# Kernel optimization log

Hardware: AMD Instinct MI355X
Metric: run time of the kernel (lower is better)

Reference implementation:

```python
import jax, jax.numpy as jnp
import numpy as np

N_CH = 128      # n_channels (out_channels)
MID = 128       # mid_channels
NF = 16         # num_filters
N_NODES = 50000


def _omeg():
    i = jnp.arange(NF, dtype=jnp.float32)
    return (10.0 * N_CH ** (1.0 - 2.0 * i / NF)).reshape(1, NF)


def setup_inputs() -> dict:
    key = jax.random.key(0)
    ks = jax.random.split(key, 16)
    E = 800000
    inp = {
        "x": jax.random.normal(ks[0], (N_NODES, N_CH), jnp.float32),
        "edge_index": jax.random.randint(ks[1], (2, E), 0, N_NODES, jnp.int64),
        "edge_attr": jax.random.normal(ks[2], (E, N_CH), jnp.float32),
        "x_pos": jax.random.normal(ks[3], (N_NODES, 3), jnp.float32),
    }
    def lin(k, fan_in, fan_out):
        kw, kb = jax.random.split(k)
        bound = 1.0 / np.sqrt(fan_in)
        w = jax.random.uniform(kw, (fan_in, fan_out), jnp.float32, -bound, bound)
        b = jax.random.uniform(kb, (fan_out,), jnp.float32, -bound, bound)
        return w, b
    inp["w1"], inp["b1"] = lin(ks[4], N_CH, N_CH)          # atomwise1
    inp["mw1"], inp["mb1"] = lin(ks[5], 2 * NF + 2 * N_CH, MID)  # message MLP
    inp["mw2"], inp["mb2"] = lin(ks[6], MID, MID)
    inp["mw3"], inp["mb3"] = lin(ks[7], MID, N_CH)
    inp["w2"], inp["b2"] = lin(ks[8], N_CH, N_CH)          # atomwise2
    inp["w3"], inp["b3"] = lin(ks[9], N_CH, N_CH)          # atomwise3
    return inp


def reference(x, edge_index, edge_attr, x_pos, w1, b1, mw1, mb1, mw2, mb2, mw3, mb3, w2, b2, w3, b3):
    h = x @ w1 + b1                                   # atomwise1 [N, C]
    src, dst = edge_index[0], edge_index[1]           # PyG: x_j = src, x_i = dst
    r = jnp.linalg.norm(x_pos[dst] - x_pos[src], axis=-1, keepdims=True)  # [E,1], p=2
    feat = r * _omeg()                                # [E, NF]
    msg_in = jnp.concatenate([jnp.sin(feat), jnp.cos(feat), edge_attr, h[src]], axis=-1)
    m = jax.nn.gelu(msg_in @ mw1 + mb1, approximate=False)
    m = jax.nn.gelu(m @ mw2 + mb2, approximate=False)
    m = m @ mw3 + mb3                                 # dropout is identity at eval
    agg = jax.ops.segment_sum(m, dst, num_segments=N_NODES)
    h = h + agg                                       # residual in cfconv
    out = jax.nn.relu(h @ w2 + b2) @ w3 + b3
    return out
```

## Files before the change

kernel.cpp:

```cpp
#include <hip/hip_runtime.h>
#include <math.h>

#define NCH 128
#define TE 64
#define TF 32
#define AP 296
#define AF 132
#define XP 136

typedef __attribute__((ext_vector_type(8))) _Float16 half8;
typedef __attribute__((ext_vector_type(4))) _Float16 half4;
typedef __attribute__((ext_vector_type(4))) float f32x4;

__device__ __forceinline__ float gelu_exact(float v) {
    return 0.5f * v * (1.0f + erff(v * 0.70710678118654752f));
}

__device__ __forceinline__ float erf_fast(float x) {
    float ax = fabsf(x);
    float t  = __builtin_amdgcn_rcpf(fmaf(0.3275911f, ax, 1.0f));
    float p  = fmaf(t, 1.061405429f, -1.453152027f);
    p = fmaf(t, p, 1.421413741f);
    p = fmaf(t, p, -0.284496736f);
    p = fmaf(t, p, 0.254829592f);
    float e  = exp2f(-ax * ax * 1.4426950408889634f);
    float r  = fmaf(-p * t, e, 1.0f);
    return copysignf(r, x);
}

__device__ __forceinline__ float gelu_fast(float v) {
    return 0.5f * v * (1.0f + erf_fast(v * 0.70710678118654752f));
}

__device__ __forceinline__ half4 cvt4(float4 v) {
#if __has_builtin(__builtin_amdgcn_cvt_pkrtz)
    auto a = __builtin_amdgcn_cvt_pkrtz(v.x, v.y);
    auto b = __builtin_amdgcn_cvt_pkrtz(v.z, v.w);
    half4 r;
    r[0] = a[0]; r[1] = a[1]; r[2] = b[0]; r[3] = b[1];
    return r;
#else
    return (half4){(_Float16)v.x, (_Float16)v.y, (_Float16)v.z, (_Float16)v.w};
#endif
}

__device__ __forceinline__ void sincos_rev(float rev, float* s, float* c) {
    float fr = rev - floorf(rev);
#if __has_builtin(__builtin_amdgcn_sinf) && __has_builtin(__builtin_amdgcn_cosf)
    *s = __builtin_amdgcn_sinf(fr);
    *c = __builtin_amdgcn_cosf(fr);
#else
    float rad = fr * 6.283185307179586f;
    *s = sinf(rad);
    *c = cosf(rad);
#endif
}

__global__ __launch_bounds__(256) void k_hist(const int* __restrict__ ei,
                                              int* __restrict__ cnt, int E) {
    int e = blockIdx.x * 256 + threadIdx.x;
    if (e < E) atomicAdd(&cnt[ei[E + e]], 1);
}

__global__ __launch_bounds__(256) void k_scan_local(const int* __restrict__ cnt,
                                                    int* __restrict__ fill,
                                                    int* __restrict__ bsum, int n) {
    __shared__ int sdata[256];
    const int tid = threadIdx.x;
    const int i = blockIdx.x * 256 + tid;
    int v = (i < n) ? cnt[i] : 0;
    sdata[tid] = v;
    __syncthreads();
    #pragma unroll
    for (int off = 1; off < 256; off <<= 1) {
        int t = (tid >= off) ? sdata[tid - off] : 0;
        __syncthreads();
        sdata[tid] += t;
        __syncthreads();
    }
    if (i < n) fill[i] = sdata[tid] - v;
    if (tid == 255) bsum[blockIdx.x] = sdata[255];
}

__global__ __launch_bounds__(256) void k_scan_bsum(int* __restrict__ bsum, int nb) {
    __shared__ int sdata[256];
    const int tid = threadIdx.x;
    int v = (tid < nb) ? bsum[tid] : 0;
    sdata[tid] = v;
    __syncthreads();
    #pragma unroll
    for (int off = 1; off < 256; off <<= 1) {
        int t = (tid >= off) ? sdata[tid - off] : 0;
        __syncthreads();
        sdata[tid] += t;
        __syncthreads();
    }
    if (tid < nb) bsum[tid] = sdata[tid] - v;
}

__global__ __launch_bounds__(256) void k_scan_add(int* __restrict__ fill,
                                                  const int* __restrict__ bsum, int n) {
    int i = blockIdx.x * 256 + threadIdx.x;
    if (i < n) fill[i] += bsum[blockIdx.x];
}

__global__ __launch_bounds__(256) void k_scan_serial(const int* __restrict__ cnt,
                                                     int* __restrict__ fill, int n) {
    __shared__ int sdata[256];
    __shared__ int carry;
    const int tid = threadIdx.x;
    if (tid == 0) carry = 0;
    __syncthreads();
    for (int base = 0; base < n; base += 256) {
        int i = base + tid;
        int v = (i < n) ? cnt[i] : 0;
        sdata[tid] = v;
        __syncthreads();
        #pragma unroll
        for (int off = 1; off < 256; off <<= 1) {
            int t = (tid >= off) ? sdata[tid - off] : 0;
            __syncthreads();
            sdata[tid] += t;
            __syncthreads();
        }
        int incl = sdata[tid];
        if (i < n) fill[i] = incl - v + carry;
        __syncthreads();
        if (tid == 255) carry += incl;
        __syncthreads();
    }
}

__global__ __launch_bounds__(256) void k_permute(const int* __restrict__ ei,
                                                 int* __restrict__ fill,
                                                 int* __restrict__ perm, int E) {
    int e = blockIdx.x * 256 + threadIdx.x;
    if (e < E) {
        int d = ei[E + e];
        int slot = atomicAdd(&fill[d], 1);
        perm[slot] = e;
    }
}

__global__ __launch_bounds__(256) void k_prep_all(
    const float* __restrict__ mw1, const float* __restrict__ mw2,
    const float* __restrict__ mw3, const float* __restrict__ w1,
    const float* __restrict__ w2, const float* __restrict__ w3,
    _Float16* __restrict__ wf, _Float16* __restrict__ awf,
    _Float16* __restrict__ o2f, _Float16* __restrict__ o3f)
{
    int b = blockIdx.x;
    const float* W; _Float16* out; int nch;
    if      (b < 18) { W = mw1; out = wf;             nch = 9; }
    else if (b < 26) { W = mw2; out = wf + 9 * 4096;  nch = 4; b -= 18; }
    else if (b < 34) { W = mw3; out = wf + 13 * 4096; nch = 4; b -= 26; }
    else if (b < 42) { W = w1;  out = awf;            nch = 4; b -= 34; }
    else if (b < 50) { W = w2;  out = o2f;            nch = 4; b -= 42; }
    else             { W = w3;  out = o3f;            nch = 4; b -= 50; }
    int idx = b * 256 + threadIdx.x;
    if (idx >= nch * 512) return;
    int c    = idx >> 9;
    int r    = idx & 511;
    int wv   = r >> 7;
    int nf   = (r >> 6) & 1;
    int lane = r & 63;
    int n  = wv * 32 + nf * 16 + (lane & 15);
    int k0 = c * 32 + (lane >> 4) * 8;
    half8 v;
    #pragma unroll
    for (int j = 0; j < 8; ++j) v[j] = (_Float16)W[(size_t)(k0 + j) * NCH + n];
    *(half8*)(out + (size_t)idx * 8) = v;
}

__global__ __launch_bounds__(256, 4) void k_aw1_mfma(
    const float* __restrict__ x, const _Float16* __restrict__ awf,
    const float* __restrict__ b1, float* __restrict__ h,
    _Float16* __restrict__ h2, int N)
{
    __shared__ __align__(16) _Float16 Xs[64][XP];

    const int tid  = threadIdx.x;
    const int row0 = blockIdx.x * 64;
    const int lane = tid & 63;
    const int w    = tid >> 6;
    const int lrow = lane & 15;
    const int lk8  = lane >> 4;
    const int n0   = w * 32;

    const half8* bp = (const half8*)awf + (w * 128 + lane);
    half8 b[2][2];
    b[0][0] = bp[0];   b[0][1] = bp[64];
    b[1][0] = bp[512]; b[1][1] = bp[512 + 64];

    #pragma unroll
    for (int t = 0; t < 8; ++t) {
        int idx = tid + t * 256;
        int r = idx >> 5, f4 = idx & 31;
        int gr = row0 + r;
        float4 v = {0.f, 0.f, 0.f, 0.f};
        if (gr < N) v = *(const float4*)(x + (size_t)gr * NCH + f4 * 4);
        *(half4*)&Xs[r][f4 * 4] = cvt4(v);
    }
    __syncthreads();

    f32x4 acc[4][2];
    #pragma unroll
    for (int mb = 0; mb < 4; ++mb)
        #pragma unroll
        for (int nf = 0; nf < 2; ++nf) acc[mb][nf] = (f32x4){0.f, 0.f, 0.f, 0.f};

    #pragma unroll
    for (int i = 0; i < 4; ++i) {
        const int s = i & 1;
        half8 av[4];
        #pragma unroll
        for (int mb = 0; mb < 4; ++mb)
            av[mb] = *(const half8*)&Xs[mb * 16 + lrow][i * 32 + lk8 * 8];
        #pragma unroll
        for (int mb = 0; mb < 4; ++mb) {
            acc[mb][0] = __builtin_amdgcn_mfma_f32_16x16x32_f16(av[mb], b[s][0], acc[mb][0], 0, 0, 0);
            acc[mb][1] = __builtin_amdgcn_mfma_f32_16x16x32_f16(av[mb], b[s][1], acc[mb][1], 0, 0, 0);
        }
        if (i + 2 < 4) {
            b[s][0] = bp[(size_t)(i + 2) * 512];
            b[s][1] = bp[(size_t)(i + 2) * 512 + 64];
        }
    }

    float bi0 = b1[n0 + lrow], bi1 = b1[n0 + 16 + lrow];
    #pragma unroll
    for (int mb = 0; mb < 4; ++mb)
        #pragma unroll
        for (int q = 0; q < 4; ++q) {
            int gr = row0 + mb * 16 + lk8 * 4 + q;
            if (gr < N) {
                float v0 = acc[mb][0][q] + bi0;
                float v1 = acc[mb][1][q] + bi1;
                h[(size_t)gr * NCH + n0 + lrow]       = v0;
                h[(size_t)gr * NCH + n0 + 16 + lrow]  = v1;
                h2[(size_t)gr * NCH + n0 + lrow]      = (_Float16)v0;
                h2[(size_t)gr * NCH + n0 + 16 + lrow] = (_Float16)v1;
            }
        }
}

__global__ __launch_bounds__(256, 8) void k_edges_mfma(
    const int* __restrict__ ei, const float* __restrict__ eattr,
    const float* __restrict__ xpos, const _Float16* __restrict__ h2,
    float* h,
    const int* __restrict__ perm,
    const _Float16* __restrict__ wf,
    const float* __restrict__ mb1, const float* __restrict__ mb2,
    const float* __restrict__ mb3, int E)
{
    __shared__ __align__(16) _Float16 As[TF][AP];
    __shared__ int permS[TF], dstS[TF];

    const int tid  = threadIdx.x;
    const int e0   = blockIdx.x * TF;
    const int lane = tid & 63;
    const int w    = tid >> 6;
    const int lrow = lane & 15;
    const int lk8  = lane >> 4;
    const int n0   = w * 32;

    const half8* bp = (const half8*)wf + (w * 128 + lane);
    half8 b[2][2];
    b[0][0] = bp[0];   b[0][1] = bp[64];
    b[1][0] = bp[512]; b[1][1] = bp[512 + 64];

    if (tid < TF) {
        int ge = e0 + tid;
        int pe = (ge < E) ? perm[ge] : -1;
        permS[tid] = pe;
        dstS[tid]  = (pe >= 0) ? ei[E + pe] : -1;
    }
    __syncthreads();

    float4 ea[4];
    #pragma unroll
    for (int t = 0; t < 4; ++t) {
        int idx = tid + t * 256;
        int pe = permS[idx >> 5];
        ea[t] = (pe >= 0) ? *(const float4*)(eattr + (size_t)pe * NCH + (idx & 31) * 4)
                          : (float4){0.f, 0.f, 0.f, 0.f};
    }
    uint4 hv[2];
    #pragma unroll
    for (int t = 0; t < 2; ++t) {
        int idx = tid + t * 256;
        int pe = permS[idx >> 4];
        int s = (pe >= 0) ? ei[pe] : 0;
        hv[t] = *(const uint4*)(h2 + (size_t)s * NCH + (idx & 15) * 8);
    }

    {
        int le = tid >> 3, i0 = tid & 7;
        int pe = permS[le];
        float r = 0.f;
        if (pe >= 0) {
            int s = ei[pe], d = dstS[le];
            float dx = xpos[d * 3 + 0] - xpos[s * 3 + 0];
            float dy = xpos[d * 3 + 1] - xpos[s * 3 + 1];
            float dz = xpos[d * 3 + 2] - xpos[s * 3 + 2];
            r = sqrtf(dx * dx + dy * dy + dz * dz);
        }
        #pragma unroll
        for (int u = 0; u < 2; ++u) {
            int i = i0 + u * 8;
            float omr = 1.5915494309f * exp2f(7.0f - 0.875f * (float)i);
            float sv, cv;
            sincos_rev(r * omr, &sv, &cv);
            As[le][i]      = (_Float16)sv;
            As[le][16 + i] = (_Float16)cv;
        }
    }
    #pragma unroll
    for (int t = 0; t < 4; ++t) {
        int idx = tid + t * 256;
        *(half4*)&As[idx >> 5][32 + (idx & 31) * 4] = cvt4(ea[t]);
    }
    #pragma unroll
    for (int t = 0; t < 2; ++t) {
        int idx = tid + t * 256;
        *(uint4*)&As[idx >> 4][160 + (idx & 15) * 8] = hv[t];
    }
    __syncthreads();

    f32x4 acc[2][2];
    #pragma unroll
    for (int mb = 0; mb < 2; ++mb)
        #pragma unroll
        for (int nf = 0; nf < 2; ++nf) acc[mb][nf] = (f32x4){0.f, 0.f, 0.f, 0.f};

    auto epi = [&](const float* __restrict__ mbv) {
        float bi0 = mbv[n0 + lrow], bi1 = mbv[n0 + 16 + lrow];
        #pragma unroll
        for (int mb = 0; mb < 2; ++mb)
            #pragma unroll
            for (int nf = 0; nf < 2; ++nf) {
                float bb = nf ? bi1 : bi0;
                #pragma unroll
                for (int q = 0; q < 4; ++q) {
                    float g = gelu_fast(acc[mb][nf][q] + bb);
                    As[mb * 16 + lk8 * 4 + q][n0 + nf * 16 + lrow] = (_Float16)g;
                }
                acc[mb][nf] = (f32x4){0.f, 0.f, 0.f, 0.f};
            }
    };

    #pragma unroll
    for (int i = 0; i < 17; ++i) {
        const int s  = i & 1;
        const int lc = (i < 9) ? i : (i < 13) ? (i - 9) : (i - 13);
        half8 av0 = *(const half8*)&As[lrow][lc * 32 + lk8 * 8];
        half8 av1 = *(const half8*)&As[16 + lrow][lc * 32 + lk8 * 8];
        __builtin_amdgcn_s_setprio(1);
        acc[0][0] = __builtin_amdgcn_mfma_f32_16x16x32_f16(av0, b[s][0], acc[0][0], 0, 0, 0);
        acc[0][1] = __builtin_amdgcn_mfma_f32_16x16x32_f16(av0, b[s][1], acc[0][1], 0, 0, 0);
        acc[1][0] = __builtin_amdgcn_mfma_f32_16x16x32_f16(av1, b[s][0], acc[1][0], 0, 0, 0);
        acc[1][1] = __builtin_amdgcn_mfma_f32_16x16x32_f16(av1, b[s][1], acc[1][1], 0, 0, 0);
        __builtin_amdgcn_s_setprio(0);
        if (i + 2 < 17) {
            b[s][0] = bp[(size_t)(i + 2) * 512];
            b[s][1] = bp[(size_t)(i + 2) * 512 + 64];
        }
        if (i == 8)  { __syncthreads(); epi(mb1); __syncthreads(); }
        if (i == 12) { __syncthreads(); epi(mb2); __syncthreads(); }
    }

    {
        float bi0 = mb3[n0 + lrow], bi1 = mb3[n0 + 16 + lrow];
        __syncthreads();
        float* Asf = (float*)&As[0][0];
        #pragma unroll
        for (int mb = 0; mb < 2; ++mb)
            #pragma unroll
            for (int nf = 0; nf < 2; ++nf) {
                float bb = nf ? bi1 : bi0;
                #pragma unroll
                for (int q = 0; q < 4; ++q) {
                    int e = mb * 16 + lk8 * 4 + q;
                    Asf[e * AF + n0 + nf * 16 + lrow] = acc[mb][nf][q] + bb;
                }
            }
        __syncthreads();

        const int c     = tid & 127;
        const int ebase = (tid >> 7) * 16;
        float run = 0.f;
        int prev = -1;
        #pragma unroll
        for (int le = 0; le < 16; ++le) {
            int d = __builtin_amdgcn_readfirstlane(dstS[ebase + le]);
            float v = Asf[(ebase + le) * AF + c];
            if (d != prev) {
                if (prev >= 0) atomicAdd(h + (size_t)prev * NCH + c, run);
                run = 0.f;
                prev = d;
            }
            if (d >= 0) run += v;
        }
        if (prev >= 0) atomicAdd(h + (size_t)prev * NCH + c, run);
    }
}

__global__ __launch_bounds__(256, 4) void k_out_mfma(
    const float* h, const _Float16* __restrict__ o2f,
    const float* __restrict__ b2, const _Float16* __restrict__ o3f,
    const float* __restrict__ b3, float* out, int N)
{
    __shared__ __align__(16) _Float16 Xs[64][XP];

    const int tid  = threadIdx.x;
    const int row0 = blockIdx.x * 64;
    const int lane = tid & 63;
    const int w    = tid >> 6;
    const int lrow = lane & 15;
    const int lk8  = lane >> 4;
    const int n0   = w * 32;

    const half8* bp2 = (const half8*)o2f + (w * 128 + lane);
    const half8* bp3 = (const half8*)o3f + (w * 128 + lane);
    half8 b[2][2];
    b[0][0] = bp2[0];   b[0][1] = bp2[64];
    b[1][0] = bp2[512]; b[1][1] = bp2[512 + 64];

    #pragma unroll
    for (int t = 0; t < 8; ++t) {
        int idx = tid + t * 256;
        int r = idx >> 5, f4 = idx & 31;
        int gr = row0 + r;
        float4 v = {0.f, 0.f, 0.f, 0.f};
        if (gr < N) v = *(const float4*)(h + (size_t)gr * NCH + f4 * 4);
        *(half4*)&Xs[r][f4 * 4] = cvt4(v);
    }
    __syncthreads();

    f32x4 acc[4][2];
    #pragma unroll
    for (int mb = 0; mb < 4; ++mb)
        #pragma unroll
        for (int nf = 0; nf < 2; ++nf) acc[mb][nf] = (f32x4){0.f, 0.f, 0.f, 0.f};

    #pragma unroll
    for (int i = 0; i < 4; ++i) {
        const int s = i & 1;
        half8 av[4];
        #pragma unroll
        for (int mb = 0; mb < 4; ++mb)
            av[mb] = *(const half8*)&Xs[mb * 16 + lrow][i * 32 + lk8 * 8];
        #pragma unroll
        for (int mb = 0; mb < 4; ++mb) {
            acc[mb][0] = __builtin_amdgcn_mfma_f32_16x16x32_f16(av[mb], b[s][0], acc[mb][0], 0, 0, 0);
            acc[mb][1] = __builtin_amdgcn_mfma_f32_16x16x32_f16(av[mb], b[s][1], acc[mb][1], 0, 0, 0);
        }
        if (i + 2 < 4) {
            b[s][0] = bp2[(size_t)(i + 2) * 512];
            b[s][1] = bp2[(size_t)(i + 2) * 512 + 64];
        } else {
            b[s][0] = bp3[(size_t)(i - 2) * 512];
            b[s][1] = bp3[(size_t)(i - 2) * 512 + 64];
        }
    }
    __syncthreads();

    {
        float bi0 = b2[n0 + lrow], bi1 = b2[n0 + 16 + lrow];
        #pragma unroll
        for (int mb = 0; mb < 4; ++mb)
            #pragma unroll
            for (int nf = 0; nf < 2; ++nf) {
                float bb = nf ? bi1 : bi0;
                #pragma unroll
                for (int q = 0; q < 4; ++q) {
                    float g = fmaxf(acc[mb][nf][q] + bb, 0.f);
                    Xs[mb * 16 + lk8 * 4 + q][n0 + nf * 16 + lrow] = (_Float16)g;
                }
                acc[mb][nf] = (f32x4){0.f, 0.f, 0.f, 0.f};
            }
    }
    __syncthreads();

    #pragma unroll
    for (int i = 0; i < 4; ++i) {
        const int s = i & 1;
        half8 av[4];
        #pragma unroll
        for (int mb = 0; mb < 4; ++mb)
            av[mb] = *(const half8*)&Xs[mb * 16 + lrow][i * 32 + lk8 * 8];
        #pragma unroll
        for (int mb = 0; mb < 4; ++mb) {
            acc[mb][0] = __builtin_amdgcn_mfma_f32_16x16x32_f16(av[mb], b[s][0], acc[mb][0], 0, 0, 0);
            acc[mb][1] = __builtin_amdgcn_mfma_f32_16x16x32_f16(av[mb], b[s][1], acc[mb][1], 0, 0, 0);
        }
        if (i + 2 < 4) {
            b[s][0] = bp3[(size_t)(i + 2) * 512];
            b[s][1] = bp3[(size_t)(i + 2) * 512 + 64];
        }
    }

    float bi0 = b3[n0 + lrow], bi1 = b3[n0 + 16 + lrow];
    #pragma unroll
    for (int mb = 0; mb < 4; ++mb)
        #pragma unroll
        for (int q = 0; q < 4; ++q) {
            int gr = row0 + mb * 16 + lk8 * 4 + q;
            if (gr < N) {
                out[(size_t)gr * NCH + n0 + lrow]      = acc[mb][0][q] + bi0;
                out[(size_t)gr * NCH + n0 + 16 + lrow] = acc[mb][1][q] + bi1;
            }
        }
}

__global__ __launch_bounds__(256) void k_atomwise1(
    const float* __restrict__ x, const float* __restrict__ w1,
    const float* __restrict__ b1, float* __restrict__ h,
    float* __restrict__ h2, int N)
{
    __shared__ float xs[16][NCH];
    const int row0 = blockIdx.x * 16;
    const int tid = threadIdx.x;
    #pragma unroll
    for (int t = 0; t < 8; ++t) {
        int idx = tid + t * 256;
        int r = idx >> 7, c = idx & 127;
        int gr = row0 + r;
        xs[r][c] = (gr < N) ? x[(size_t)gr * NCH + c] : 0.f;
    }
    __syncthreads();
    const int j = tid & 127;
    const int rg = tid >> 7;
    float acc[8];
    #pragma unroll
    for (int i = 0; i < 8; ++i) acc[i] = 0.f;
    for (int k = 0; k < NCH; ++k) {
        float wv = w1[(size_t)k * NCH + j];
        #pragma unroll
        for (int i = 0; i < 8; ++i)
            acc[i] = fmaf(xs[rg * 8 + i][k], wv, acc[i]);
    }
    float bv = b1[j];
    #pragma unroll
    for (int i = 0; i < 8; ++i) {
        int gr = row0 + rg * 8 + i;
        if (gr < N) {
            float v = acc[i] + bv;
            h[(size_t)gr * NCH + j]  = v;
            h2[(size_t)gr * NCH + j] = v;
        }
    }
}

__global__ __launch_bounds__(256) void k_edges_f32(
    const int* __restrict__ ei, const float* __restrict__ eattr,
    const float* __restrict__ xpos, const float* __restrict__ h,
    const float* __restrict__ mw1, const float* __restrict__ mb1,
    const float* __restrict__ mw2, const float* __restrict__ mb2,
    const float* __restrict__ mw3, const float* __restrict__ mb3,
    float* __restrict__ agg, int E)
{
    __shared__ __align__(16) float Asf[TE][292];
    __shared__ float Wsf[32][NCH];
    __shared__ int srcS[TE];
    __shared__ int dstS[TE];
    const int tid = threadIdx.x;
    const int e0 = blockIdx.x * TE;
    if (tid < TE) {
        int e = e0 + tid;
        int s = 0, d = -1;
        float r = 0.f;
        if (e < E) {
            s = ei[e]; d = ei[E + e];
            float dx = xpos[d * 3 + 0] - xpos[s * 3 + 0];
            float dy = xpos[d * 3 + 1] - xpos[s * 3 + 1];
            float dz = xpos[d * 3 + 2] - xpos[s * 3 + 2];
            r = sqrtf(dx * dx + dy * dy + dz * dz);
        }
        srcS[tid] = s; dstS[tid] = d;
        #pragma unroll
        for (int i = 0; i < 16; ++i) {
            float om = 10.f * exp2f(7.0f - 0.875f * (float)i);
            float f = r * om;
            Asf[tid][i] = sinf(f); Asf[tid][16 + i] = cosf(f);
        }
    }
    __syncthreads();
    {
        const int half = tid >> 7;
        const int c = tid & 127;
        for (int ee = 0; ee < TE; ee += 2) {
            int le = ee + half;
            int e = e0 + le;
            if (e < E) {
                Asf[le][32 + c]  = eattr[(size_t)e * NCH + c];
                Asf[le][160 + c] = h[(size_t)srcS[le] * NCH + c];
            } else { Asf[le][32 + c] = 0.f; Asf[le][160 + c] = 0.f; }
        }
    }
    const int jl = tid & 31;
    const int g  = tid >> 5;
    float acc[8][4];
    auto run_layer = [&](const float* __restrict__ Wg, int K) {
        #pragma unroll
        for (int i = 0; i < 8; ++i)
            #pragma unroll
            for (int c = 0; c < 4; ++c) acc[i][c] = 0.f;
        for (int k0 = 0; k0 < K; k0 += 32) {
            __syncthreads();
            #pragma unroll
            for (int t = 0; t < 16; ++t) {
                int idx = tid + t * 256;
                Wsf[idx >> 7][idx & 127] =
                    Wg[(size_t)(k0 + (idx >> 7)) * NCH + (idx & 127)];
            }
            __syncthreads();
            #pragma unroll
            for (int kk = 0; kk < 32; kk += 4) {
                float4 a[8];
                #pragma unroll
                for (int i = 0; i < 8; ++i)
                    a[i] = *reinterpret_cast<const float4*>(&Asf[g * 8 + i][k0 + kk]);
                #pragma unroll
                for (int u = 0; u < 4; ++u) {
                    float w0 = Wsf[kk + u][jl];
                    float w1v = Wsf[kk + u][jl + 32];
                    float w2v = Wsf[kk + u][jl + 64];
                    float w3v = Wsf[kk + u][jl + 96];
                    #pragma unroll
                    for (int i = 0; i < 8; ++i) {
                        float avv = (&a[i].x)[u];
                        acc[i][0] = fmaf(avv, w0, acc[i][0]);
                        acc[i][1] = fmaf(avv, w1v, acc[i][1]);
                        acc[i][2] = fmaf(avv, w2v, acc[i][2]);
                        acc[i][3] = fmaf(avv, w3v, acc[i][3]);
                    }
                }
            }
        }
    };
    run_layer(mw1, 288);
    #pragma unroll
    for (int i = 0; i < 8; ++i)
        #pragma unroll
        for (int c = 0; c < 4; ++c) {
            int j = jl + 32 * c;
            Asf[g * 8 + i][j] = gelu_exact(acc[i][c] + mb1[j]);
        }
    run_layer(mw2, 128);
    #pragma unroll
    for (int i = 0; i < 8; ++i)
        #pragma unroll
        for (int c = 0; c < 4; ++c) {
            int j = jl + 32 * c;
            Asf[g * 8 + i][j] = gelu_exact(acc[i][c] + mb2[j]);
        }
    run_layer(mw3, 128);
    #pragma unroll
    for (int i = 0; i < 8; ++i) {
        int d = dstS[g * 8 + i];
        if (d >= 0) {
            #pragma unroll
            for (int c = 0; c < 4; ++c) {
                int j = jl + 32 * c;
                atomicAdd(&agg[(size_t)d * NCH + j], acc[i][c] + mb3[j]);
            }
        }
    }
}

__global__ __launch_bounds__(256) void k_out(
    const float* h, const float* aggOpt,
    const float* __restrict__ w2, const float* __restrict__ b2,
    const float* __restrict__ w3, const float* __restrict__ b3,
    float* out, int N)
{
    __shared__ float hs[16][NCH];
    __shared__ float ts[16][NCH];
    const int row0 = blockIdx.x * 16;
    const int tid = threadIdx.x;
    #pragma unroll
    for (int t = 0; t < 8; ++t) {
        int idx = tid + t * 256;
        int r = idx >> 7, c = idx & 127;
        int gr = row0 + r;
        float v = 0.f;
        if (gr < N) {
            v = h[(size_t)gr * NCH + c];
            if (aggOpt) v += aggOpt[(size_t)gr * NCH + c];
        }
        hs[r][c] = v;
    }
    __syncthreads();
    const int j = tid & 127;
    const int rg = tid >> 7;
    float acc[8];
    #pragma unroll
    for (int i = 0; i < 8; ++i) acc[i] = 0.f;
    for (int k = 0; k < NCH; ++k) {
        float wv = w2[(size_t)k * NCH + j];
        #pragma unroll
        for (int i = 0; i < 8; ++i)
            acc[i] = fmaf(hs[rg * 8 + i][k], wv, acc[i]);
    }
    float bv = b2[j];
    #pragma unroll
    for (int i = 0; i < 8; ++i)
        ts[rg * 8 + i][j] = fmaxf(acc[i] + bv, 0.f);
    __syncthreads();
    float acc2[8];
    #pragma unroll
    for (int i = 0; i < 8; ++i) acc2[i] = 0.f;
    for (int k = 0; k < NCH; ++k) {
        float wv = w3[(size_t)k * NCH + j];
        #pragma unroll
        for (int i = 0; i < 8; ++i)
            acc2[i] = fmaf(ts[rg * 8 + i][k], wv, acc2[i]);
    }
    float b3v = b3[j];
    #pragma unroll
    for (int i = 0; i < 8; ++i) {
        int gr = row0 + rg * 8 + i;
        if (gr < N) out[(size_t)gr * NCH + j] = acc2[i] + b3v;
    }
}

extern "C" void kernel_launch(void* const* d_in, const int* in_sizes, int n_in,
                              void* d_out, int out_size, void* d_ws, size_t ws_size,
                              hipStream_t stream)
{
    const float* x     = (const float*)d_in[0];
    const int*   ei    = (const int*)d_in[1];
    const float* eattr = (const float*)d_in[2];
    const float* xpos  = (const float*)d_in[3];
    const float* w1    = (const float*)d_in[4];
    const float* b1    = (const float*)d_in[5];
    const float* mw1   = (const float*)d_in[6];
    const float* mb1   = (const float*)d_in[7];
    const float* mw2   = (const float*)d_in[8];
    const float* mb2   = (const float*)d_in[9];
    const float* mw3   = (const float*)d_in[10];
    const float* mb3   = (const float*)d_in[11];
    const float* w2    = (const float*)d_in[12];
    const float* b2    = (const float*)d_in[13];
    const float* w3    = (const float*)d_in[14];
    const float* b3    = (const float*)d_in[15];

    const int N = in_sizes[0] / NCH;
    const int E = in_sizes[1] / 2;

    float* h = (float*)d_out;

    const int nbscan = (N + 255) / 256;
    const size_t h2_bytes = (size_t)N * NCH * sizeof(_Float16);
    const size_t wchunks  = 17 + 4 + 4 + 4;
    const size_t wbytes   = wchunks * 4096 * sizeof(_Float16);
    const size_t csr_bytes = ((size_t)2 * N + E + nbscan) * sizeof(int);
    const bool fast = ws_size >= h2_bytes + wbytes + csr_bytes;

    if (fast) {
        _Float16* h2  = (_Float16*)d_ws;
        _Float16* wf  = (_Float16*)((char*)d_ws + h2_bytes);
        _Float16* awf = wf + 17 * 4096;
        _Float16* o2f = awf + 4 * 4096;
        _Float16* o3f = o2f + 4 * 4096;
        int* cnt  = (int*)(o3f + 4 * 4096);
        int* fill = cnt + N;
        int* perm = fill + N;
        int* bsum = perm + E;

        hipMemsetAsync(cnt, 0, (size_t)N * sizeof(int), stream);
        k_hist<<<(E + 255) / 256, 256, 0, stream>>>(ei, cnt, E);
        if (nbscan <= 256) {
            k_scan_local<<<nbscan, 256, 0, stream>>>(cnt, fill, bsum, N);
            k_scan_bsum<<<1, 256, 0, stream>>>(bsum, nbscan);
            k_scan_add<<<nbscan, 256, 0, stream>>>(fill, bsum, N);
        } else {
            k_scan_serial<<<1, 256, 0, stream>>>(cnt, fill, N);
        }
        k_permute<<<(E + 255) / 256, 256, 0, stream>>>(ei, fill, perm, E);

        k_prep_all<<<58, 256, 0, stream>>>(mw1, mw2, mw3, w1, w2, w3,
                                           wf, awf, o2f, o3f);
        const int nb = (N + 63) / 64;
        k_aw1_mfma<<<nb, 256, 0, stream>>>(x, awf, b1, h, h2, N);
        k_edges_mfma<<<(E + TF - 1) / TF, 256, 0, stream>>>(
            ei, eattr, xpos, h2, h, perm, wf, mb1, mb2, mb3, E);
        k_out_mfma<<<nb, 256, 0, stream>>>(h, o2f, b2, o3f, b3, (float*)d_out, N);
    } else {
        float* agg = (float*)d_ws;
        k_atomwise1<<<(N + 15) / 16, 256, 0, stream>>>(x, w1, b1, h, agg, N);
        hipMemsetAsync(agg, 0, (size_t)N * NCH * sizeof(float), stream);
        k_edges_f32<<<(E + TE - 1) / TE, 256, 0, stream>>>(
            ei, eattr, xpos, h, mw1, mb1, mw2, mb2, mw3, mb3, agg, E);
        k_out<<<(N + 15) / 16, 256, 0, stream>>>(h, agg, w2, b2, w3, b3,
                                                 (float*)d_out, N);
    }
}
```

Before: 396.0 us.

## Double edge tile to 64 per block and fold scan offset into permute

The edge MLP kernel now processes 64 edges per block instead of 32, so each wave issues four M-blocks of MFMAs per loaded weight fragment. This halves the weight reloads per edge and the number of blocks. Occupancy is lowered to 4 blocks per CU to fit the larger register and LDS footprint. Separately, the scan-add kernel is removed and the block offset is added inside a new permute kernel, which saves one launch and one pass over the fill array.

```diff
diff --git a/kernel.cpp b/kernel.cpp
--- a/kernel.cpp
+++ b/kernel.cpp
@@ -3,7 +3,7 @@
 
 #define NCH 128
 #define TE 64
-#define TF 32
+#define TF 64
 #define AP 296
 #define AF 132
 #define XP 136
@@ -98,12 +98,6 @@
     if (tid < nb) bsum[tid] = sdata[tid] - v;
 }
 
-__global__ __launch_bounds__(256) void k_scan_add(int* __restrict__ fill,
-                                                  const int* __restrict__ bsum, int n) {
-    int i = blockIdx.x * 256 + threadIdx.x;
-    if (i < n) fill[i] += bsum[blockIdx.x];
-}
-
 __global__ __launch_bounds__(256) void k_scan_serial(const int* __restrict__ cnt,
                                                      int* __restrict__ fill, int n) {
     __shared__ int sdata[256];
@@ -128,6 +122,18 @@
         __syncthreads();
         if (tid == 255) carry += incl;
         __syncthreads();
+    }
+}
+
+__global__ __launch_bounds__(256) void k_permute_off(const int* __restrict__ ei,
+                                                     int* __restrict__ fill,
+                                                     const int* __restrict__ bsum,
+                                                     int* __restrict__ perm, int E) {
+    int e = blockIdx.x * 256 + threadIdx.x;
+    if (e < E) {
+        int d = ei[E + e];
+        int slot = bsum[d >> 8] + atomicAdd(&fill[d], 1);
+        perm[slot] = e;
     }
 }
 
@@ -244,7 +250,7 @@
         }
 }
 
-__global__ __launch_bounds__(256, 8) void k_edges_mfma(
+__global__ __launch_bounds__(256, 4) void k_edges_mfma(
     const int* __restrict__ ei, const float* __restrict__ eattr,
     const float* __restrict__ xpos, const _Float16* __restrict__ h2,
     float* h,
@@ -277,17 +283,17 @@
     }
     __syncthreads();
 
-    float4 ea[4];
-    #pragma unroll
-    for (int t = 0; t < 4; ++t) {
+    float4 ea[8];
+    #pragma unroll
+    for (int t = 0; t < 8; ++t) {
         int idx = tid + t * 256;
         int pe = permS[idx >> 5];
         ea[t] = (pe >= 0) ? *(const float4*)(eattr + (size_t)pe * NCH + (idx & 31) * 4)
                           : (float4){0.f, 0.f, 0.f, 0.f};
     }
-    uint4 hv[2];
-    #pragma unroll
-    for (int t = 0; t < 2; ++t) {
+    uint4 hv[4];
+    #pragma unroll
+    for (int t = 0; t < 4; ++t) {
         int idx = tid + t * 256;
         int pe = permS[idx >> 4];
         int s = (pe >= 0) ? ei[pe] : 0;
@@ -295,7 +301,7 @@
     }
 
     {
-        int le = tid >> 3, i0 = tid & 7;
+        int le = tid >> 2, i0 = tid & 3;
         int pe = permS[le];
         float r = 0.f;
         if (pe >= 0) {
@@ -306,8 +312,8 @@
             r = sqrtf(dx * dx + dy * dy + dz * dz);
         }
         #pragma unroll
-        for (int u = 0; u < 2; ++u) {
-            int i = i0 + u * 8;
+        for (int u = 0; u < 4; ++u) {
+            int i = i0 + u * 4;
             float omr = 1.5915494309f * exp2f(7.0f - 0.875f * (float)i);
             float sv, cv;
             sincos_rev(r * omr, &sv, &cv);
@@ -316,27 +322,27 @@
         }
     }
     #pragma unroll
+    for (int t = 0; t < 8; ++t) {
+        int idx = tid + t * 256;
+        *(half4*)&As[idx >> 5][32 + (idx & 31) * 4] = cvt4(ea[t]);
+    }
+    #pragma unroll
     for (int t = 0; t < 4; ++t) {
         int idx = tid + t * 256;
-        *(half4*)&As[idx >> 5][32 + (idx & 31) * 4] = cvt4(ea[t]);
-    }
-    #pragma unroll
-    for (int t = 0; t < 2; ++t) {
-        int idx = tid + t * 256;
         *(uint4*)&As[idx >> 4][160 + (idx & 15) * 8] = hv[t];
     }
     __syncthreads();
 
-    f32x4 acc[2][2];
-    #pragma unroll
-    for (int mb = 0; mb < 2; ++mb)
+    f32x4 acc[4][2];
+    #pragma unroll
+    for (int mb = 0; mb < 4; ++mb)
         #pragma unroll
         for (int nf = 0; nf < 2; ++nf) acc[mb][nf] = (f32x4){0.f, 0.f, 0.f, 0.f};
 
     auto epi = [&](const float* __restrict__ mbv) {
         float bi0 = mbv[n0 + lrow], bi1 = mbv[n0 + 16 + lrow];
         #pragma unroll
-        for (int mb = 0; mb < 2; ++mb)
+        for (int mb = 0; mb < 4; ++mb)
             #pragma unroll
             for (int nf = 0; nf < 2; ++nf) {
                 float bb = nf ? bi1 : bi0;
@@ -353,13 +359,16 @@
     for (int i = 0; i < 17; ++i) {
         const int s  = i & 1;
         const int lc = (i < 9) ? i : (i < 13) ? (i - 9) : (i - 13);
-        half8 av0 = *(const half8*)&As[lrow][lc * 32 + lk8 * 8];
-        half8 av1 = *(const half8*)&As[16 + lrow][lc * 32 + lk8 * 8];
+        half8 av[4];
+        #pragma unroll
+        for (int mb = 0; mb < 4; ++mb)
+            av[mb] = *(const half8*)&As[mb * 16 + lrow][lc * 32 + lk8 * 8];
         __builtin_amdgcn_s_setprio(1);
-        acc[0][0] = __builtin_amdgcn_mfma_f32_16x16x32_f16(av0, b[s][0], acc[0][0], 0, 0, 0);
-        acc[0][1] = __builtin_amdgcn_mfma_f32_16x16x32_f16(av0, b[s][1], acc[0][1], 0, 0, 0);
-        acc[1][0] = __builtin_amdgcn_mfma_f32_16x16x32_f16(av1, b[s][0], acc[1][0], 0, 0, 0);
-        acc[1][1] = __builtin_amdgcn_mfma_f32_16x16x32_f16(av1, b[s][1], acc[1][1], 0, 0, 0);
+        #pragma unroll
+        for (int mb = 0; mb < 4; ++mb) {
+            acc[mb][0] = __builtin_amdgcn_mfma_f32_16x16x32_f16(av[mb], b[s][0], acc[mb][0], 0, 0, 0);
+            acc[mb][1] = __builtin_amdgcn_mfma_f32_16x16x32_f16(av[mb], b[s][1], acc[mb][1], 0, 0, 0);
+        }
         __builtin_amdgcn_s_setprio(0);
         if (i + 2 < 17) {
             b[s][0] = bp[(size_t)(i + 2) * 512];
@@ -374,7 +383,7 @@
         __syncthreads();
         float* Asf = (float*)&As[0][0];
         #pragma unroll
-        for (int mb = 0; mb < 2; ++mb)
+        for (int mb = 0; mb < 4; ++mb)
             #pragma unroll
             for (int nf = 0; nf < 2; ++nf) {
                 float bb = nf ? bi1 : bi0;
@@ -387,11 +396,11 @@
         __syncthreads();
 
         const int c     = tid & 127;
-        const int ebase = (tid >> 7) * 16;
+        const int ebase = (tid >> 7) * 32;
         float run = 0.f;
         int prev = -1;
         #pragma unroll
-        for (int le = 0; le < 16; ++le) {
+        for (int le = 0; le < 32; ++le) {
             int d = __builtin_amdgcn_readfirstlane(dstS[ebase + le]);
             float v = Asf[(ebase + le) * AF + c];
             if (d != prev) {
@@ -774,11 +783,11 @@
         if (nbscan <= 256) {
             k_scan_local<<<nbscan, 256, 0, stream>>>(cnt, fill, bsum, N);
             k_scan_bsum<<<1, 256, 0, stream>>>(bsum, nbscan);
-            k_scan_add<<<nbscan, 256, 0, stream>>>(fill, bsum, N);
+            k_permute_off<<<(E + 255) / 256, 256, 0, stream>>>(ei, fill, bsum, perm, E);
         } else {
             k_scan_serial<<<1, 256, 0, stream>>>(cnt, fill, N);
-        }
-        k_permute<<<(E + 255) / 256, 256, 0, stream>>>(ei, fill, perm, E);
+            k_permute<<<(E + 255) / 256, 256, 0, stream>>>(ei, fill, perm, E);
+        }
 
         k_prep_all<<<58, 256, 0, stream>>>(mw1, mw2, mw3, w1, w2, w3,
                                            wf, awf, o2f, o3f);
```

Measured after the change: 399.9 us. No clear change (+1.0%).
